# Kernel tuning notes

Measured on AMD Instinct MI355X. Metric: run time of the kernel, lower is better.

Reference implementation:

```python
import jax, jax.numpy as jnp
import numpy as np

GRID_SIZE = 5
ORDER = 3  # spline_order
H_STEP = 2.0 / GRID_SIZE  # grid_range = [-1, 1]
GRID = jnp.arange(-ORDER, GRID_SIZE + ORDER + 1, dtype=jnp.float32) * H_STEP - 1.0  # (12,)


def b_splines(x):
    # x: (N, F) -> bases: (N, F, GRID_SIZE + ORDER) via Cox-de Boor recursion
    g = GRID
    xx = x[..., None]
    bases = ((xx >= g[:-1]) & (xx < g[1:])).astype(x.dtype)
    for k in range(1, ORDER + 1):
        left = (xx - g[:-(k + 1)]) / (g[k:-1] - g[:-(k + 1)]) * bases[..., :-1]
        right = (g[k + 1:] - xx) / (g[k + 1:] - g[1:-k]) * bases[..., 1:]
        bases = left + right
    return bases


def kan_linear(x, bw, sw, sc):
    # x: (N, F); bw: (O, F); sw: (O, F, C); sc: (O, F)
    base = jax.nn.silu(x) @ bw.T
    spline = jnp.einsum('nfc,ofc->no', b_splines(x), sw * sc[..., None])
    return base + spline


def kan_conv(x, bw, sw, sc):
    # x: (B, C, H, W); 3x3 patches, padding 1, stride 1 -> KANLinear over C*9 features
    B, C, H, W = x.shape
    patches = jax.lax.conv_general_dilated_patches(x, (3, 3), (1, 1), ((1, 1), (1, 1)))  # (B, C*9, H, W)
    p = patches.transpose(0, 2, 3, 1).reshape(B * H * W, C * 9)
    o = kan_linear(p, bw, sw, sc)  # (B*H*W, Cout)
    return o.reshape(B, H, W, -1).transpose(0, 3, 1, 2)


def maxpool2(x):
    B, C, H, W = x.shape
    return x.reshape(B, C, H // 2, 2, W // 2, 2).max(axis=(3, 5))


def setup_inputs() -> dict:
    key = jax.random.key(0)
    ks = jax.random.split(key, 32)
    d = {}
    d['x'] = jax.random.normal(ks[0], (128, 3, 32, 32), dtype=jnp.float32)
    conv_specs = [(3, 4), (4, 8), (8, 16), (16, 32)]
    i = 1
    for li, (cin, cout) in enumerate(conv_specs, 1):
        fin = cin * 9
        d[f'bw{li}'] = jax.random.normal(ks[i], (cout, fin), dtype=jnp.float32) * (1.0 / np.sqrt(fin)); i += 1
        d[f'sw{li}'] = jax.random.normal(ks[i], (cout, fin, GRID_SIZE + ORDER), dtype=jnp.float32) * 0.1; i += 1
        d[f'sc{li}'] = jax.random.normal(ks[i], (cout, fin), dtype=jnp.float32) * (1.0 / np.sqrt(fin)); i += 1
    lin_specs = [(2048, 2048), (1024, 2048), (10, 1024)]
    for li, (o, inn) in enumerate(lin_specs, 1):
        d[f'w{li}'] = jax.random.normal(ks[i], (o, inn), dtype=jnp.float32) * (1.0 / np.sqrt(inn)); i += 1
        d[f'b{li}'] = jnp.zeros((o,), dtype=jnp.float32); i += 1
    return d


def reference(x, bw1, sw1, sc1, bw2, sw2, sc2, bw3, sw3, sc3, bw4, sw4, sc4, w1, b1, w2, b2, w3, b3):
    x = kan_conv(x, bw1, sw1, sc1)
    x = kan_conv(x, bw2, sw2, sc2)
    x = maxpool2(x)
    x = kan_conv(x, bw3, sw3, sc3)
    x = kan_conv(x, bw4, sw4, sc4)
    x = maxpool2(x)
    x = x.reshape(x.shape[0], -1)  # (B, 32*8*8)
    x = jax.nn.relu(x @ w1.T + b1)
    x = jax.nn.relu(x @ w2.T + b2)
    return x @ w3.T + b3
```

## Files before the change

### kernel.cpp

```cpp
#include <hip/hip_runtime.h>
#include <hip/hip_bf16.h>

#define BATCH 128
#define AST 88

typedef __attribute__((ext_vector_type(8))) short bf16x8;
typedef __attribute__((ext_vector_type(16))) float f32x16;

__device__ __forceinline__ void spline_acts(float xv, float act[9]) {
    act[0] = xv * (1.0f / (1.0f + __expf(-xv)));
    float g[12];
#pragma unroll
    for (int i = 0; i < 12; ++i) g[i] = (float)(i - 3) * 0.4f - 1.0f;
    float bb[11];
#pragma unroll
    for (int c = 0; c < 11; ++c) bb[c] = (xv >= g[c] && xv < g[c + 1]) ? 1.0f : 0.0f;
#pragma unroll
    for (int k = 1; k <= 3; ++k) {
#pragma unroll
        for (int c = 0; c + k < 11; ++c) {
            float left  = (xv - g[c]) * (1.0f / (g[c + k] - g[c])) * bb[c];
            float right = (g[c + k + 1] - xv) * (1.0f / (g[c + k + 1] - g[c + 1])) * bb[c + 1];
            bb[c] = left + right;
        }
    }
#pragma unroll
    for (int c = 0; c < 8; ++c) act[c + 1] = bb[c];
}

__device__ __constant__ float ZPAD[9] = {0.0f, 0.0f, 0.0f, 0.02083333333f,
                                         0.47916666667f, 0.47916666667f,
                                         0.02083333333f, 0.0f, 0.0f};

__device__ __forceinline__ void bf16split(float x, ushort& h, ushort& l) {
    __hip_bfloat16 bh = __float2bfloat16(x);
    float hf = __bfloat162float(bh);
    __hip_bfloat16 bl = __float2bfloat16(x - hf);
    h = *(ushort*)&bh;
    l = *(ushort*)&bl;
}

__device__ __forceinline__ float wval(const float* bw, const float* sw, const float* sc,
                                      int F, int f, int j, int o) {
    if (j == 0) return bw[o * F + f];
    return sw[(o * F + f) * 8 + (j - 1)] * sc[o * F + f];
}

__global__ __launch_bounds__(256) void prep_kernel(
    const float* __restrict__ bw1, const float* __restrict__ sw1, const float* __restrict__ sc1,
    const float* __restrict__ bw2, const float* __restrict__ sw2, const float* __restrict__ sc2,
    const float* __restrict__ bw3, const float* __restrict__ sw3, const float* __restrict__ sc3,
    const float* __restrict__ bw4, const float* __restrict__ sw4, const float* __restrict__ sc4,
    ushort* __restrict__ k1h, ushort* __restrict__ k1l,
    ushort* __restrict__ k2h, ushort* __restrict__ k2l,
    ushort* __restrict__ k3h, ushort* __restrict__ k3l,
    ushort* __restrict__ k4h, ushort* __restrict__ k4l,
    ushort* __restrict__ zph, ushort* __restrict__ zpl) {
    int i = blockIdx.x * 256 + threadIdx.x;
    if (i < 1152) {
        int l = i & 63, s = (i >> 6) & 1, t = i / 128;
#pragma unroll
        for (int e = 0; e < 8; ++e) {
            int k = s * 16 + ((l >> 5) * 8) + e, o = l & 31;
            float w = 0.f;
            if (k < 27 && o < 4) w = wval(bw1, sw1, sc1, 27, (k / 9) * 9 + t, k % 9, o);
            ushort h, lo; bf16split(w, h, lo);
            k1h[i * 8 + e] = h; k1l[i * 8 + e] = lo;
        }
    } else if (i < 2880) {
        int q = i - 1152;
        int l = q & 63, s = (q >> 6) % 3, t = q / 192;
#pragma unroll
        for (int e = 0; e < 8; ++e) {
            int k = s * 16 + ((l >> 5) * 8) + e, o = l & 31;
            float w = 0.f;
            if (k < 36 && o < 8) w = wval(bw2, sw2, sc2, 36, (k / 9) * 9 + t, k % 9, o);
            ushort h, lo; bf16split(w, h, lo);
            k2h[q * 8 + e] = h; k2l[q * 8 + e] = lo;
        }
    } else if (i < 5760) {
        int q = i - 2880;
        int l = q & 63, s = (q >> 6) % 5, t = q / 320;
#pragma unroll
        for (int e = 0; e < 8; ++e) {
            int k = s * 16 + ((l >> 5) * 8) + e, o = l & 31;
            float w = 0.f;
            if (k < 72 && o < 16) w = wval(bw3, sw3, sc3, 72, (k / 9) * 9 + t, k % 9, o);
            ushort h, lo; bf16split(w, h, lo);
            k3h[q * 8 + e] = h; k3l[q * 8 + e] = lo;
        }
    } else if (i < 11520) {
        int q = i - 5760;
        int l = q & 63, s = (q >> 6) % 5, t = (q / 320) % 9, p = q / 2880;
#pragma unroll
        for (int e = 0; e < 8; ++e) {
            int k = s * 16 + ((l >> 5) * 8) + e, o = l & 31;
            float w = 0.f;
            if (k < 72) w = wval(bw4, sw4, sc4, 144, (p * 8 + k / 9) * 9 + t, k % 9, o);
            ushort h, lo; bf16split(w, h, lo);
            k4h[q * 8 + e] = h; k4l[q * 8 + e] = lo;
        }
    } else if (i < 11600) {
        int c = i - 11520;
        ushort h, lo; bf16split(ZPAD[c % 9], h, lo);
        zph[c] = h; zpl[c] = lo;
    }
}

__global__ __launch_bounds__(256) void conv1_fused(
    const float* __restrict__ x,
    const ushort* __restrict__ Bgh, const ushort* __restrict__ Bgl,
    ushort* __restrict__ Oh, ushort* __restrict__ Ol) {
    constexpr int ASTR = 32, KSTEPS = 2, NCO = 4;
    __shared__ ushort AH[340 * ASTR];
    __shared__ ushort AL[340 * ASTR];
    const int tid = threadIdx.x;
    const int b = blockIdx.x >> 2, strip = blockIdx.x & 3;
    const int r0 = strip * 8;
    const int lane = tid & 63, wv = tid >> 6;

    for (int px = tid; px < 340; px += 256) {
        int lr = px / 34, pc = px - lr * 34;
        int grow = r0 - 1 + lr, gc = pc - 1;
        bool inb = ((unsigned)grow < 32u) && ((unsigned)gc < 32u);
        unsigned rh[16], rl[16];
#pragma unroll
        for (int w = 0; w < 16; ++w) { rh[w] = 0u; rl[w] = 0u; }
        if (inb) {
            const float* xb = x + (size_t)b * 3072 + grow * 32 + gc;
#pragma unroll
            for (int cin = 0; cin < 3; ++cin) {
                float a9[9];
                spline_acts(xb[cin * 1024], a9);
#pragma unroll
                for (int j = 0; j < 9; ++j) {
                    ushort h, l2; bf16split(a9[j], h, l2);
                    int c = cin * 9 + j;
                    if (c & 1) { rh[c >> 1] |= (unsigned)h << 16; rl[c >> 1] |= (unsigned)l2 << 16; }
                    else       { rh[c >> 1] |= h;                  rl[c >> 1] |= l2; }
                }
            }
        } else {
#pragma unroll
            for (int c = 0; c < 27; ++c) {
                ushort h, l2; bf16split(ZPAD[c % 9], h, l2);
                if (c & 1) { rh[c >> 1] |= (unsigned)h << 16; rl[c >> 1] |= (unsigned)l2 << 16; }
                else       { rh[c >> 1] |= h;                  rl[c >> 1] |= l2; }
            }
        }
        unsigned* dh = (unsigned*)&AH[px * ASTR];
        unsigned* dl = (unsigned*)&AL[px * ASTR];
#pragma unroll
        for (int w = 0; w < 16; ++w) { dh[w] = rh[w]; dl[w] = rl[w]; }
    }
    __syncthreads();

    f32x16 acc0, acc1;
#pragma unroll
    for (int i = 0; i < 16; ++i) { acc0[i] = 0.f; acc1[i] = 0.f; }

    const int p0 = wv * 64 + (lane & 31);
    const int sp0 = ((p0 >> 5) + 1) * 34 + (p0 & 31) + 1;
    const int sp1 = sp0 + 34;
    const int koff = (lane >> 5) * 8;

#pragma unroll 1
    for (int t = 0; t < 9; ++t) {
        const int dA = ((t / 3) - 1) * 34 + (t % 3) - 1;
#pragma unroll
        for (int s = 0; s < KSTEPS; ++s) {
            bf16x8 a0h = *(const bf16x8*)(&AH[(sp0 + dA) * ASTR + s * 16 + koff]);
            bf16x8 a0l = *(const bf16x8*)(&AL[(sp0 + dA) * ASTR + s * 16 + koff]);
            bf16x8 a1h = *(const bf16x8*)(&AH[(sp1 + dA) * ASTR + s * 16 + koff]);
            bf16x8 a1l = *(const bf16x8*)(&AL[(sp1 + dA) * ASTR + s * 16 + koff]);
            bf16x8 bh = *(const bf16x8*)(Bgh + (size_t)((t * KSTEPS + s) * 64 + lane) * 8);
            bf16x8 bl = *(const bf16x8*)(Bgl + (size_t)((t * KSTEPS + s) * 64 + lane) * 8);
            acc0 = __builtin_amdgcn_mfma_f32_32x32x16_bf16(a0h, bh, acc0, 0, 0, 0);
            acc1 = __builtin_amdgcn_mfma_f32_32x32x16_bf16(a1h, bh, acc1, 0, 0, 0);
            acc0 = __builtin_amdgcn_mfma_f32_32x32x16_bf16(a0h, bl, acc0, 0, 0, 0);
            acc1 = __builtin_amdgcn_mfma_f32_32x32x16_bf16(a1h, bl, acc1, 0, 0, 0);
            acc0 = __builtin_amdgcn_mfma_f32_32x32x16_bf16(a0l, bh, acc0, 0, 0, 0);
            acc1 = __builtin_amdgcn_mfma_f32_32x32x16_bf16(a1l, bh, acc1, 0, 0, 0);
        }
    }
    __syncthreads();

    float* fl = (float*)AH;
    {
        int ccol = lane & 31;
        if (ccol < NCO) {
#pragma unroll
            for (int r = 0; r < 16; ++r) {
                int row = (r & 3) + 8 * (r >> 2) + 4 * (lane >> 5);
                fl[ccol * 257 + wv * 64 + row] = acc0[r];
                fl[ccol * 257 + wv * 64 + 32 + row] = acc1[r];
            }
        }
    }
    __syncthreads();

    unsigned* ubh = (unsigned*)AL;
    unsigned* ubl = (unsigned*)AH + 1032;
    ubl = (unsigned*)AH + 832;
    {
        unsigned rwh[18], rwl[18];
        float v4[4];
#pragma unroll
        for (int co = 0; co < 4; ++co) v4[co] = fl[co * 257 + tid];
        __syncthreads();
#pragma unroll
        for (int w = 0; w < 18; ++w) { rwh[w] = 0u; rwl[w] = 0u; }
#pragma unroll
        for (int co = 0; co < 4; ++co) {
            float a9[9];
            spline_acts(v4[co], a9);
#pragma unroll
            for (int j = 0; j < 9; ++j) {
                ushort h, l2; bf16split(a9[j], h, l2);
                int c = co * 9 + j;
                if (c & 1) { rwh[c >> 1] |= (unsigned)h << 16; rwl[c >> 1] |= (unsigned)l2 << 16; }
                else       { rwh[c >> 1] |= h;                  rwl[c >> 1] |= l2; }
            }
        }
#pragma unroll
        for (int w = 0; w < 18; ++w) { ubh[tid * 18 + w] = rwh[w]; ubl[tid * 18 + w] = rwl[w]; }
    }
    __syncthreads();
    size_t basew = ((size_t)b * 1024 + strip * 256) * 18;
    unsigned* goh = (unsigned*)Oh + basew;
    unsigned* gol = (unsigned*)Ol + basew;
#pragma unroll
    for (int e = 0; e < 18; ++e) {
        int q = e * 256 + tid;
        goh[q] = ubh[q];
        gol[q] = ubl[q];
    }
}

template <int KG, int CHG, int CHL, int ASTR, int KSTEPS, int NCO>
__global__ __launch_bounds__(256) void conv2_strip(
    const ushort* __restrict__ Agh, const ushort* __restrict__ Agl,
    const ushort* __restrict__ Bgh, const ushort* __restrict__ Bgl,
    const ushort* __restrict__ zph, const ushort* __restrict__ zpl,
    ushort* __restrict__ Oh, ushort* __restrict__ Ol) {
    __shared__ ushort AH[340 * ASTR];
    __shared__ ushort AL[340 * ASTR];
    const int tid = threadIdx.x;
    const int b = blockIdx.x >> 2, strip = blockIdx.x & 3;
    const int r0 = strip * 8;
    const int lane = tid & 63, wv = tid >> 6;

    {
        const ushort* ash = Agh + (size_t)b * 1024 * KG;
        const ushort* asl = Agl + (size_t)b * 1024 * KG;
        for (int idx = tid; idx < 320 * CHL; idx += 256) {
            int pxl = idx / CHL, ch = idx - pxl * CHL;
            int lr = pxl >> 5, c = pxl & 31;
            int grow = r0 - 1 + lr;
            uint2 vh, vl;
            if (ch >= CHG) { vh = make_uint2(0u, 0u); vl = make_uint2(0u, 0u); }
            else if ((unsigned)grow < 32u) {
                vh = *(const uint2*)(ash + (size_t)(grow * 32 + c) * KG + ch * 4);
                vl = *(const uint2*)(asl + (size_t)(grow * 32 + c) * KG + ch * 4);
            } else {
                vh = *(const uint2*)(zph + ch * 4);
                vl = *(const uint2*)(zpl + ch * 4);
            }
            int spx = lr * 34 + c + 1;
            *(uint2*)(&AH[spx * ASTR + ch * 4]) = vh;
            *(uint2*)(&AL[spx * ASTR + ch * 4]) = vl;
        }
        for (int idx = tid; idx < 20 * CHL; idx += 256) {
            int sel = idx / CHL, ch = idx - sel * CHL;
            int lr = sel >> 1, c = (sel & 1) ? 33 : 0;
            int spx = lr * 34 + c;
            uint2 vh, vl;
            if (ch >= CHG) { vh = make_uint2(0u, 0u); vl = make_uint2(0u, 0u); }
            else { vh = *(const uint2*)(zph + ch * 4); vl = *(const uint2*)(zpl + ch * 4); }
            *(uint2*)(&AH[spx * ASTR + ch * 4]) = vh;
            *(uint2*)(&AL[spx * ASTR + ch * 4]) = vl;
        }
    }
    __syncthreads();

    f32x16 acc0, acc1;
#pragma unroll
    for (int i = 0; i < 16; ++i) { acc0[i] = 0.f; acc1[i] = 0.f; }

    const int p0 = wv * 64 + (lane & 31);
    const int sp0 = ((p0 >> 5) + 1) * 34 + (p0 & 31) + 1;
    const int sp1 = sp0 + 34;
    const int koff = (lane >> 5) * 8;

#pragma unroll 1
    for (int t = 0; t < 9; ++t) {
        const int dA = ((t / 3) - 1) * 34 + (t % 3) - 1;
#pragma unroll
        for (int s = 0; s < KSTEPS; ++s) {
            bf16x8 a0h = *(const bf16x8*)(&AH[(sp0 + dA) * ASTR + s * 16 + koff]);
            bf16x8 a0l = *(const bf16x8*)(&AL[(sp0 + dA) * ASTR + s * 16 + koff]);
            bf16x8 a1h = *(const bf16x8*)(&AH[(sp1 + dA) * ASTR + s * 16 + koff]);
            bf16x8 a1l = *(const bf16x8*)(&AL[(sp1 + dA) * ASTR + s * 16 + koff]);
            bf16x8 bh = *(const bf16x8*)(Bgh + (size_t)((t * KSTEPS + s) * 64 + lane) * 8);
            bf16x8 bl = *(const bf16x8*)(Bgl + (size_t)((t * KSTEPS + s) * 64 + lane) * 8);
            acc0 = __builtin_amdgcn_mfma_f32_32x32x16_bf16(a0h, bh, acc0, 0, 0, 0);
            acc1 = __builtin_amdgcn_mfma_f32_32x32x16_bf16(a1h, bh, acc1, 0, 0, 0);
            acc0 = __builtin_amdgcn_mfma_f32_32x32x16_bf16(a0h, bl, acc0, 0, 0, 0);
            acc1 = __builtin_amdgcn_mfma_f32_32x32x16_bf16(a1h, bl, acc1, 0, 0, 0);
            acc0 = __builtin_amdgcn_mfma_f32_32x32x16_bf16(a0l, bh, acc0, 0, 0, 0);
            acc1 = __builtin_amdgcn_mfma_f32_32x32x16_bf16(a1l, bh, acc1, 0, 0, 0);
        }
    }
    __syncthreads();

    float* fl = (float*)AH;
    {
        int ccol = lane & 31;
        if (ccol < NCO) {
#pragma unroll
            for (int r = 0; r < 16; ++r) {
                int row = (r & 3) + 8 * (r >> 2) + 4 * (lane >> 5);
                fl[ccol * 257 + wv * 64 + row] = acc0[r];
                fl[ccol * 257 + wv * 64 + 32 + row] = acc1[r];
            }
        }
    }
    __syncthreads();

    int cg = tid >> 6, pl = tid & 63;
    int phl = pl >> 4, pw = pl & 15;
    int base_m = (2 * phl) * 32 + 2 * pw;
    unsigned rwh[9], rwl[9];
#pragma unroll
    for (int w = 0; w < 9; ++w) { rwh[w] = 0u; rwl[w] = 0u; }
#pragma unroll
    for (int e = 0; e < 2; ++e) {
        int co = cg * 2 + e;
        const float* fb = fl + co * 257 + base_m;
        float m = fmaxf(fmaxf(fb[0], fb[1]), fmaxf(fb[32], fb[33]));
        float a9[9];
        spline_acts(m, a9);
#pragma unroll
        for (int j = 0; j < 9; ++j) {
            ushort h, l2; bf16split(a9[j], h, l2);
            int c = e * 9 + j;
            if (c & 1) { rwh[c >> 1] |= (unsigned)h << 16; rwl[c >> 1] |= (unsigned)l2 << 16; }
            else       { rwh[c >> 1] |= h;                  rwl[c >> 1] |= l2; }
        }
    }
    unsigned* ubh = (unsigned*)AL;
    unsigned* ubl = (unsigned*)AL + 2560;
#pragma unroll
    for (int w = 0; w < 9; ++w) {
        ubh[pl * 40 + cg * 9 + w] = rwh[w];
        ubl[pl * 40 + cg * 9 + w] = rwl[w];
    }
    if (cg == 3) {
#pragma unroll
        for (int w = 0; w < 4; ++w) { ubh[pl * 40 + 36 + w] = 0u; ubl[pl * 40 + 36 + w] = 0u; }
    }
    __syncthreads();
    size_t base = ((size_t)b * 256 + strip * 64) * 80;
    const ushort* sbh = (const ushort*)ubh;
    const ushort* sbl = (const ushort*)ubl;
#pragma unroll
    for (int e = 0; e < 3; ++e) {
        int q = e * 256 + tid;
        if (q < 640) {
            *(uint4*)(Oh + base + q * 8) = *(const uint4*)(sbh + q * 8);
            *(uint4*)(Ol + base + q * 8) = *(const uint4*)(sbl + q * 8);
        }
    }
}

template <int NPH, int NCO>
__global__ __launch_bounds__(256) void conv34_part(
    const ushort* __restrict__ Agh, const ushort* __restrict__ Agl,
    const ushort* __restrict__ Bgh, const ushort* __restrict__ Bgl,
    const ushort* __restrict__ zph, const ushort* __restrict__ zpl,
    float* __restrict__ P) {
    __shared__ ushort AH[144 * AST];
    __shared__ ushort AL[144 * AST];
    const int tid = threadIdx.x;
    const int b = blockIdx.x, half = blockIdx.y, g = blockIdx.z;
    const int r0 = half * 8;
    const int lane = tid & 63, wv = tid >> 6;

    f32x16 acc;
#pragma unroll
    for (int i = 0; i < 16; ++i) acc[i] = 0.f;

    const int m = wv * 32 + (lane & 31);
    const int sbase = (m >> 4) * 18 + (m & 15);
    const int koff = (lane >> 5) * 8;

#pragma unroll 1
    for (int p = 0; p < NPH; ++p) {
        if (p) __syncthreads();
        const ushort* ash = Agh + ((size_t)b * NPH + p) * 256 * 80;
        const ushort* asl = Agl + ((size_t)b * NPH + p) * 256 * 80;
#pragma unroll
        for (int e = 0; e < 6; ++e) {
            int idx = e * 256 + tid;
            if (idx < 1440) {
                int px = idx / 10, ch = idx - px * 10;
                int pr = px / 18, pc = px - pr * 18;
                int r = r0 - 1 + g + pr, c = pc - 1;
                bool inb = ((unsigned)r < 16u) && ((unsigned)c < 16u);
                uint4 vh, vl;
                if (inb) {
                    vh = *(const uint4*)(ash + (size_t)(r * 16 + c) * 80 + ch * 8);
                    vl = *(const uint4*)(asl + (size_t)(r * 16 + c) * 80 + ch * 8);
                } else {
                    vh = *(const uint4*)(zph + ch * 8);
                    vl = *(const uint4*)(zpl + ch * 8);
                }
                *(uint4*)(&AH[px * AST + ch * 8]) = vh;
                *(uint4*)(&AL[px * AST + ch * 8]) = vl;
            }
        }
        __syncthreads();

        const ushort* bsh = Bgh + (size_t)p * 2880 * 8;
        const ushort* bsl = Bgl + (size_t)p * 2880 * 8;
#pragma unroll
        for (int dw = 0; dw < 3; ++dw) {
            const int t = g * 3 + dw;
#pragma unroll
            for (int s = 0; s < 5; ++s) {
                bf16x8 ah = *(const bf16x8*)(&AH[(sbase + dw) * AST + s * 16 + koff]);
                bf16x8 al = *(const bf16x8*)(&AL[(sbase + dw) * AST + s * 16 + koff]);
                bf16x8 bh = *(const bf16x8*)(bsh + (size_t)((t * 5 + s) * 64 + lane) * 8);
                bf16x8 bl = *(const bf16x8*)(bsl + (size_t)((t * 5 + s) * 64 + lane) * 8);
                acc = __builtin_amdgcn_mfma_f32_32x32x16_bf16(ah, bh, acc, 0, 0, 0);
                acc = __builtin_amdgcn_mfma_f32_32x32x16_bf16(ah, bl, acc, 0, 0, 0);
                acc = __builtin_amdgcn_mfma_f32_32x32x16_bf16(al, bh, acc, 0, 0, 0);
            }
        }
    }

    int co = lane & 31;
    if (co < NCO) {
        float* pb = P + ((size_t)(g * 256 + b * 2 + half) * 128) * NCO;
#pragma unroll
        for (int r = 0; r < 16; ++r) {
            int px = wv * 32 + (r & 3) + 8 * (r >> 2) + 4 * (lane >> 5);
            pb[px * NCO + co] = acc[r];
        }
    }
}

__global__ __launch_bounds__(256) void conv3_reduce(const float* __restrict__ P3,
                                                    ushort* __restrict__ A4h,
                                                    ushort* __restrict__ A4l) {
    __shared__ ushort SBH[2][64 * 80];
    __shared__ ushort SBL[2][64 * 80];
    int b = blockIdx.x, pxq = blockIdx.y;
    int t = threadIdx.x;
    int co = t & 15, pxg = t >> 4;
#pragma unroll
    for (int q = 0; q < 4; ++q) {
        int lpx64 = pxg * 4 + q;
        int px = pxq * 64 + lpx64;
        int bh = b * 2 + (px >> 7), lpx = px & 127;
        float s = 0.f;
#pragma unroll
        for (int zz = 0; zz < 3; ++zz)
            s += P3[((size_t)(zz * 256 + bh) * 128 + lpx) * 16 + co];
        float a9[9];
        spline_acts(s, a9);
        int ph = co >> 3, c8 = co & 7;
#pragma unroll
        for (int j = 0; j < 9; ++j) {
            ushort h, l2; bf16split(a9[j], h, l2);
            SBH[ph][lpx64 * 80 + c8 * 9 + j] = h;
            SBL[ph][lpx64 * 80 + c8 * 9 + j] = l2;
        }
        if (c8 == 7) {
#pragma unroll
            for (int w = 0; w < 8; ++w) {
                SBH[ph][lpx64 * 80 + 72 + w] = 0;
                SBL[ph][lpx64 * 80 + 72 + w] = 0;
            }
        }
    }
    __syncthreads();
#pragma unroll
    for (int ph = 0; ph < 2; ++ph) {
        size_t base = ((size_t)(b * 2 + ph) * 256 + pxq * 64) * 80;
#pragma unroll
        for (int e = 0; e < 3; ++e) {
            int q = e * 256 + t;
            if (q < 640) {
                *(uint4*)(A4h + base + q * 8) = *(const uint4*)(&SBH[ph][q * 8]);
                *(uint4*)(A4l + base + q * 8) = *(const uint4*)(&SBL[ph][q * 8]);
            }
        }
    }
}

__global__ __launch_bounds__(256) void conv4_reduce_pool(const float* __restrict__ P4,
                                                         float* __restrict__ pooled) {
    __shared__ float SM[32 * 33];
    int b = blockIdx.x, half = blockIdx.y;
    int t = threadIdx.x;
    int co = t & 31, pg = t >> 5;
    int bh = b * 2 + half;
#pragma unroll
    for (int q = 0; q < 4; ++q) {
        int pp = pg * 4 + q;
        int lr = pp >> 3, pc = pp & 7;
        int px00 = (2 * lr) * 16 + 2 * pc;
        float s00 = 0.f, s01 = 0.f, s10 = 0.f, s11 = 0.f;
#pragma unroll
        for (int zz = 0; zz < 3; ++zz) {
            const float* pb = P4 + ((size_t)(zz * 256 + bh) * 128) * 32 + co;
            s00 += pb[(size_t)px00 * 32];
            s01 += pb[(size_t)(px00 + 1) * 32];
            s10 += pb[(size_t)(px00 + 16) * 32];
            s11 += pb[(size_t)(px00 + 17) * 32];
        }
        SM[co * 33 + pp] = fmaxf(fmaxf(s00, s01), fmaxf(s10, s11));
    }
    __syncthreads();
#pragma unroll
    for (int e = 0; e < 4; ++e) {
        int idx = e * 256 + t;
        int co2 = idx >> 5, pp2 = idx & 31;
        int lr2 = pp2 >> 3, pc2 = pp2 & 7;
        pooled[(size_t)b * 2048 + co2 * 64 + (half * 4 + lr2) * 8 + pc2] = SM[co2 * 33 + pp2];
    }
}

template <int SPLIT>
__global__ __launch_bounds__(256) void fc_big(const float* __restrict__ A,
                                              const float* __restrict__ Wt,
                                              float* __restrict__ part,
                                              int M, int N, int K) {
    __shared__ float As[32][68];
    __shared__ float Ws[32][68];
    const int tid = threadIdx.x;
    const int tx = tid & 15, ty = tid >> 4;
    const int bm = blockIdx.y * 64, bn = blockIdx.x * 64;
    const int kc = K / SPLIT;
    const int kbeg = blockIdx.z * kc;
    float acc[4][4] = {};
    for (int k0 = kbeg; k0 < kbeg + kc; k0 += 32) {
#pragma unroll
        for (int e = 0; e < 2; ++e) {
            int q = e * 256 + tid;
            int r = q >> 3, k4 = (q & 7) * 4;
            float4 av = *(const float4*)&A[(size_t)(bm + r) * K + k0 + k4];
            float4 wv = *(const float4*)&Wt[(size_t)(bn + r) * K + k0 + k4];
            As[k4 + 0][r] = av.x; As[k4 + 1][r] = av.y;
            As[k4 + 2][r] = av.z; As[k4 + 3][r] = av.w;
            Ws[k4 + 0][r] = wv.x; Ws[k4 + 1][r] = wv.y;
            Ws[k4 + 2][r] = wv.z; Ws[k4 + 3][r] = wv.w;
        }
        __syncthreads();
#pragma unroll
        for (int kk = 0; kk < 32; ++kk) {
            float4 av = *(const float4*)(&As[kk][ty * 4]);
            float4 wv = *(const float4*)(&Ws[kk][tx * 4]);
            acc[0][0] = fmaf(av.x, wv.x, acc[0][0]);
            acc[0][1] = fmaf(av.x, wv.y, acc[0][1]);
            acc[0][2] = fmaf(av.x, wv.z, acc[0][2]);
            acc[0][3] = fmaf(av.x, wv.w, acc[0][3]);
            acc[1][0] = fmaf(av.y, wv.x, acc[1][0]);
            acc[1][1] = fmaf(av.y, wv.y, acc[1][1]);
            acc[1][2] = fmaf(av.y, wv.z, acc[1][2]);
            acc[1][3] = fmaf(av.y, wv.w, acc[1][3]);
            acc[2][0] = fmaf(av.z, wv.x, acc[2][0]);
            acc[2][1] = fmaf(av.z, wv.y, acc[2][1]);
            acc[2][2] = fmaf(av.z, wv.z, acc[2][2]);
            acc[2][3] = fmaf(av.z, wv.w, acc[2][3]);
            acc[3][0] = fmaf(av.w, wv.x, acc[3][0]);
            acc[3][1] = fmaf(av.w, wv.y, acc[3][1]);
            acc[3][2] = fmaf(av.w, wv.z, acc[3][2]);
            acc[3][3] = fmaf(av.w, wv.w, acc[3][3]);
        }
        __syncthreads();
    }
    float* p = part + (size_t)blockIdx.z * M * N;
#pragma unroll
    for (int i = 0; i < 4; ++i) {
        float4 v = make_float4(acc[i][0], acc[i][1], acc[i][2], acc[i][3]);
        *(float4*)&p[(size_t)(bm + ty * 4 + i) * N + (bn + tx * 4)] = v;
    }
}

template <int SPLIT>
__global__ void fc_reduce(const float* __restrict__ part, const float* __restrict__ bias,
                          float* __restrict__ C, int MN, int N, int relu) {
    int i = blockIdx.x * 256 + threadIdx.x;
    if (i >= MN) return;
    float s = bias[i % N];
#pragma unroll
    for (int z = 0; z < SPLIT; ++z) s += part[(size_t)z * MN + i];
    C[i] = relu ? fmaxf(s, 0.f) : s;
}

__global__ __launch_bounds__(256) void fc3_kernel(const float* __restrict__ A,
                                                  const float* __restrict__ Wt,
                                                  const float* __restrict__ bias,
                                                  float* __restrict__ C) {
    int gid = blockIdx.x * 256 + threadIdx.x;
    int wid = gid >> 6;
    int lane = gid & 63;
    int m = wid / 10, n = wid - m * 10;
    const float4* a = (const float4*)(A + (size_t)m * 1024);
    const float4* w = (const float4*)(Wt + (size_t)n * 1024);
    float s = 0.f;
#pragma unroll
    for (int it = 0; it < 4; ++it) {
        float4 av = a[it * 64 + lane];
        float4 wv = w[it * 64 + lane];
        s += av.x * wv.x + av.y * wv.y + av.z * wv.z + av.w * wv.w;
    }
#pragma unroll
    for (int off = 32; off; off >>= 1) s += __shfl_xor(s, off);
    if (lane == 0) C[wid] = s + bias[n];
}

extern "C" void kernel_launch(void* const* d_in, const int* in_sizes, int n_in,
                              void* d_out, int out_size, void* d_ws, size_t ws_size,
                              hipStream_t stream) {
    const float* x   = (const float*)d_in[0];
    const float* bw1 = (const float*)d_in[1];
    const float* sw1 = (const float*)d_in[2];
    const float* sc1 = (const float*)d_in[3];
    const float* bw2 = (const float*)d_in[4];
    const float* sw2 = (const float*)d_in[5];
    const float* sc2 = (const float*)d_in[6];
    const float* bw3 = (const float*)d_in[7];
    const float* sw3 = (const float*)d_in[8];
    const float* sc3 = (const float*)d_in[9];
    const float* bw4 = (const float*)d_in[10];
    const float* sw4 = (const float*)d_in[11];
    const float* sc4 = (const float*)d_in[12];
    const float* w1  = (const float*)d_in[13];
    const float* b1  = (const float*)d_in[14];
    const float* w2  = (const float*)d_in[15];
    const float* b2  = (const float*)d_in[16];
    const float* w3  = (const float*)d_in[17];
    const float* b3  = (const float*)d_in[18];

    float*  wsf = (float*)d_ws;
    ushort* wsu = (ushort*)d_ws;
    ushort* k1h = wsu + 110848;
    ushort* k1l = wsu + 120064;
    ushort* k2h = wsu + 129280;
    ushort* k2l = wsu + 143104;
    ushort* k3h = wsu + 156928;
    ushort* k3l = wsu + 179968;
    ushort* k4h = wsu + 203008;
    ushort* k4l = wsu + 249088;
    ushort* zph = wsu + 295168;
    ushort* zpl = wsu + 295248;
    ushort* A2h = wsu + 7864320;
    ushort* A2l = wsu + 12582912;
    ushort* A3h = wsu + 524288;
    ushort* A3l = wsu + 3145728;
    ushort* A4h = wsu + 5767168;
    ushort* A4l = wsu + 11010048;
    float* P3   = wsf + 9437184;
    float* P4   = wsf + 11534336;
    float* pooled = wsf + 262144;
    float* part1  = wsf + 524288;
    float* fc1o   = wsf + 2621440;
    float* part2  = wsf + 2883584;
    float* fc2o   = wsf + 3932160;

    prep_kernel<<<46, 256, 0, stream>>>(bw1, sw1, sc1, bw2, sw2, sc2,
                                        bw3, sw3, sc3, bw4, sw4, sc4,
                                        k1h, k1l, k2h, k2l, k3h, k3l, k4h, k4l,
                                        zph, zpl);

    conv1_fused<<<512, 256, 0, stream>>>(x, k1h, k1l, A2h, A2l);
    conv2_strip<36, 9, 12, 56, 3, 8><<<512, 256, 0, stream>>>(A2h, A2l, k2h, k2l,
                                                              zph, zpl, A3h, A3l);
    conv34_part<1, 16><<<dim3(128, 2, 3), 256, 0, stream>>>(A3h, A3l, k3h, k3l,
                                                            zph, zpl, P3);
    conv3_reduce<<<dim3(128, 4), 256, 0, stream>>>(P3, A4h, A4l);
    conv34_part<2, 32><<<dim3(128, 2, 3), 256, 0, stream>>>(A4h, A4l, k4h, k4l,
                                                            zph, zpl, P4);
    conv4_reduce_pool<<<dim3(128, 2), 256, 0, stream>>>(P4, pooled);

    fc_big<8><<<dim3(32, 2, 8), 256, 0, stream>>>(pooled, w1, part1, 128, 2048, 2048);
    fc_reduce<8><<<1024, 256, 0, stream>>>(part1, b1, fc1o, 262144, 2048, 1);
    fc_big<8><<<dim3(16, 2, 8), 256, 0, stream>>>(fc1o, w2, part2, 128, 1024, 2048);
    fc_reduce<8><<<512, 256, 0, stream>>>(part2, b2, fc2o, 131072, 1024, 1);
    fc3_kernel<<<320, 256, 0, stream>>>(fc2o, w3, b3, (float*)d_out);
}
```

Baseline: 130.7 us.

## Split conv1 into 4-row strips with one MFMA tile per wave

conv1_fused now processes 4-row strips instead of 8, doubling the grid to 1024 blocks. Each wave computes one 32-pixel accumulator tile instead of two. The LDS activation stride is padded from 32 to 40 to reduce bank conflicts. The epilogue spline expansion is split across two threads per pixel (two output channels each). The aim is more parallelism and occupancy, paid for with more halo recomputation per block and a larger share of redundant spline work on the halo rows.

```diff
diff --git a/kernel.cpp b/kernel.cpp
--- a/kernel.cpp
+++ b/kernel.cpp
@@ -111,15 +111,15 @@
     const float* __restrict__ x,
     const ushort* __restrict__ Bgh, const ushort* __restrict__ Bgl,
     ushort* __restrict__ Oh, ushort* __restrict__ Ol) {
-    constexpr int ASTR = 32, KSTEPS = 2, NCO = 4;
-    __shared__ ushort AH[340 * ASTR];
-    __shared__ ushort AL[340 * ASTR];
+    constexpr int ASTR = 40, KSTEPS = 2, NCO = 4;
+    __shared__ ushort AH[204 * ASTR];
+    __shared__ ushort AL[204 * ASTR];
     const int tid = threadIdx.x;
-    const int b = blockIdx.x >> 2, strip = blockIdx.x & 3;
-    const int r0 = strip * 8;
+    const int b = blockIdx.x >> 3, strip = blockIdx.x & 7;
+    const int r0 = strip * 4;
     const int lane = tid & 63, wv = tid >> 6;
 
-    for (int px = tid; px < 340; px += 256) {
+    for (int px = tid; px < 204; px += 256) {
         int lr = px / 34, pc = px - lr * 34;
         int grow = r0 - 1 + lr, gc = pc - 1;
         bool inb = ((unsigned)grow < 32u) && ((unsigned)gc < 32u);
@@ -155,13 +155,12 @@
     }
     __syncthreads();
 
-    f32x16 acc0, acc1;
-#pragma unroll
-    for (int i = 0; i < 16; ++i) { acc0[i] = 0.f; acc1[i] = 0.f; }
-
-    const int p0 = wv * 64 + (lane & 31);
+    f32x16 acc;
+#pragma unroll
+    for (int i = 0; i < 16; ++i) acc[i] = 0.f;
+
+    const int p0 = wv * 32 + (lane & 31);
     const int sp0 = ((p0 >> 5) + 1) * 34 + (p0 & 31) + 1;
-    const int sp1 = sp0 + 34;
     const int koff = (lane >> 5) * 8;
 
 #pragma unroll 1
@@ -169,18 +168,13 @@
         const int dA = ((t / 3) - 1) * 34 + (t % 3) - 1;
 #pragma unroll
         for (int s = 0; s < KSTEPS; ++s) {
-            bf16x8 a0h = *(const bf16x8*)(&AH[(sp0 + dA) * ASTR + s * 16 + koff]);
-            bf16x8 a0l = *(const bf16x8*)(&AL[(sp0 + dA) * ASTR + s * 16 + koff]);
-            bf16x8 a1h = *(const bf16x8*)(&AH[(sp1 + dA) * ASTR + s * 16 + koff]);
-            bf16x8 a1l = *(const bf16x8*)(&AL[(sp1 + dA) * ASTR + s * 16 + koff]);
+            bf16x8 ah = *(const bf16x8*)(&AH[(sp0 + dA) * ASTR + s * 16 + koff]);
+            bf16x8 al = *(const bf16x8*)(&AL[(sp0 + dA) * ASTR + s * 16 + koff]);
             bf16x8 bh = *(const bf16x8*)(Bgh + (size_t)((t * KSTEPS + s) * 64 + lane) * 8);
             bf16x8 bl = *(const bf16x8*)(Bgl + (size_t)((t * KSTEPS + s) * 64 + lane) * 8);
-            acc0 = __builtin_amdgcn_mfma_f32_32x32x16_bf16(a0h, bh, acc0, 0, 0, 0);
-            acc1 = __builtin_amdgcn_mfma_f32_32x32x16_bf16(a1h, bh, acc1, 0, 0, 0);
-            acc0 = __builtin_amdgcn_mfma_f32_32x32x16_bf16(a0h, bl, acc0, 0, 0, 0);
-            acc1 = __builtin_amdgcn_mfma_f32_32x32x16_bf16(a1h, bl, acc1, 0, 0, 0);
-            acc0 = __builtin_amdgcn_mfma_f32_32x32x16_bf16(a0l, bh, acc0, 0, 0, 0);
-            acc1 = __builtin_amdgcn_mfma_f32_32x32x16_bf16(a1l, bh, acc1, 0, 0, 0);
+            acc = __builtin_amdgcn_mfma_f32_32x32x16_bf16(ah, bh, acc, 0, 0, 0);
+            acc = __builtin_amdgcn_mfma_f32_32x32x16_bf16(ah, bl, acc, 0, 0, 0);
+            acc = __builtin_amdgcn_mfma_f32_32x32x16_bf16(al, bh, acc, 0, 0, 0);
         }
     }
     __syncthreads();
@@ -192,8 +186,7 @@
 #pragma unroll
             for (int r = 0; r < 16; ++r) {
                 int row = (r & 3) + 8 * (r >> 2) + 4 * (lane >> 5);
-                fl[ccol * 257 + wv * 64 + row] = acc0[r];
-                fl[ccol * 257 + wv * 64 + 32 + row] = acc1[r];
+                fl[ccol * 129 + wv * 32 + row] = acc[r];
             }
         }
     }
@@ -201,36 +194,36 @@
 
     unsigned* ubh = (unsigned*)AL;
     unsigned* ubl = (unsigned*)AH + 1032;
-    ubl = (unsigned*)AH + 832;
     {
-        unsigned rwh[18], rwl[18];
-        float v4[4];
-#pragma unroll
-        for (int co = 0; co < 4; ++co) v4[co] = fl[co * 257 + tid];
-        __syncthreads();
-#pragma unroll
-        for (int w = 0; w < 18; ++w) { rwh[w] = 0u; rwl[w] = 0u; }
-#pragma unroll
-        for (int co = 0; co < 4; ++co) {
+        int px = tid >> 1, cop = tid & 1;
+        unsigned rwh[9], rwl[9];
+#pragma unroll
+        for (int w = 0; w < 9; ++w) { rwh[w] = 0u; rwl[w] = 0u; }
+#pragma unroll
+        for (int e = 0; e < 2; ++e) {
+            int co = cop * 2 + e;
             float a9[9];
-            spline_acts(v4[co], a9);
+            spline_acts(fl[co * 129 + px], a9);
 #pragma unroll
             for (int j = 0; j < 9; ++j) {
                 ushort h, l2; bf16split(a9[j], h, l2);
-                int c = co * 9 + j;
+                int c = e * 9 + j;
                 if (c & 1) { rwh[c >> 1] |= (unsigned)h << 16; rwl[c >> 1] |= (unsigned)l2 << 16; }
                 else       { rwh[c >> 1] |= h;                  rwl[c >> 1] |= l2; }
             }
         }
 #pragma unroll
-        for (int w = 0; w < 18; ++w) { ubh[tid * 18 + w] = rwh[w]; ubl[tid * 18 + w] = rwl[w]; }
-    }
-    __syncthreads();
-    size_t basew = ((size_t)b * 1024 + strip * 256) * 18;
+        for (int w = 0; w < 9; ++w) {
+            ubh[px * 18 + cop * 9 + w] = rwh[w];
+            ubl[px * 18 + cop * 9 + w] = rwl[w];
+        }
+    }
+    __syncthreads();
+    size_t basew = ((size_t)b * 1024 + strip * 128) * 18;
     unsigned* goh = (unsigned*)Oh + basew;
     unsigned* gol = (unsigned*)Ol + basew;
 #pragma unroll
-    for (int e = 0; e < 18; ++e) {
+    for (int e = 0; e < 9; ++e) {
         int q = e * 256 + tid;
         goh[q] = ubh[q];
         gol[q] = ubl[q];
@@ -676,7 +669,7 @@
                                         k1h, k1l, k2h, k2l, k3h, k3l, k4h, k4l,
                                         zph, zpl);
 
-    conv1_fused<<<512, 256, 0, stream>>>(x, k1h, k1l, A2h, A2l);
+    conv1_fused<<<1024, 256, 0, stream>>>(x, k1h, k1l, A2h, A2l);
     conv2_strip<36, 9, 12, 56, 3, 8><<<512, 256, 0, stream>>>(A2h, A2l, k2h, k2l,
                                                               zph, zpl, A3h, A3l);
     conv34_part<1, 16><<<dim3(128, 2, 3), 256, 0, stream>>>(A3h, A3l, k3h, k3l,
```

After: 129.2 us (median of 2 runs). Within noise of the previous version (-1.1%).
